# Performance work log

Measured on AMD Instinct MI355X. Metric: run time of the kernel, lower is better.

Reference implementation:

```python
import jax, jax.numpy as jnp
import numpy as np
import math

IN_C, OUT_C, KH, KW = 128, 128, 3, 3
GROUPS_NUM, NUM_W = 8, 8
STRIDE, PAD, DIL = 1, 1, 1
BETA = 1.0


def setup_inputs() -> dict:
    key = jax.random.key(0)
    ks = jax.random.split(key, 6)
    B, H, W = 8, 56, 56
    n = IN_C * KH * KW
    bound = math.sqrt(6.0 / n)  # reset_parameters bound for weight templates
    inputs = jax.random.normal(ks[0], (B, IN_C, H, W), jnp.float32)
    mask = jax.random.randint(ks[1], (B, H, W), 0, GROUPS_NUM)
    Alpha = jax.random.uniform(ks[2], (B, GROUPS_NUM, H, W), jnp.float32)
    weight_templates = jax.random.uniform(ks[3], (OUT_C * IN_C * KH * KW, NUM_W), jnp.float32, -bound, bound)
    routing_w = jax.random.normal(ks[4], (GROUPS_NUM * NUM_W, IN_C), jnp.float32) * 0.01
    routing_b = jnp.zeros((GROUPS_NUM * NUM_W,), jnp.float32)
    bias = jnp.zeros((OUT_C,), jnp.float32)
    return dict(inputs=inputs, mask=mask, Alpha=Alpha, weight_templates=weight_templates,
                routing_w=routing_w, routing_b=routing_b, bias=bias, use_alpha=1)


def _unfold(x):
    # torch F.unfold-compatible im2col: [B, C*KH*KW, Ho, Wo], channel-major feature order
    return jax.lax.conv_general_dilated_patches(
        x, (KH, KW), (STRIDE, STRIDE), [(PAD, PAD), (PAD, PAD)],
        rhs_dilation=(DIL, DIL), dimension_numbers=('NCHW', 'OIHW', 'NCHW'))


def reference(inputs, mask, Alpha, weight_templates, routing_w, routing_b, bias, use_alpha):
    B, C, H, W = inputs.shape
    K = IN_C * KH * KW
    # SE-style routing: GAP -> fc -> scaled sigmoid (alpha=1.0 in source)
    x_se = inputs.reshape(B, C, -1).mean(-1)                              # [B, C]
    x_se = 2.0 * jax.nn.sigmoid(x_se @ routing_w.T + routing_b) / NUM_W   # [B, G*num_W]
    # blend weight templates: F.linear(x_se.reshape(-1,num_W), weight)
    w = x_se.reshape(B * GROUPS_NUM, NUM_W) @ weight_templates.T          # [B*G, O*K]
    w = w.reshape(B, GROUPS_NUM, OUT_C, K).transpose(0, 2, 3, 1)          # [B, O, K, G]
    patches = _unfold(inputs)                                             # [B, K, Ho, Wo]
    # per-group convolution outputs, then per-pixel group routing
    y = jnp.einsum('bokg,bkhw->boghw', w, patches)                        # [B, O, G, Ho, Wo]
    if use_alpha:
        probs = jax.nn.softmax(BETA * Alpha, axis=1)                      # soft routing [B, G, Ho, Wo]
    else:
        probs = jax.nn.one_hot(mask, GROUPS_NUM, axis=1, dtype=y.dtype)   # hard per-pixel group select
    out = jnp.einsum('boghw,bghw->bohw', y, probs)
    return out + bias.reshape(1, -1, 1, 1)
```

## Files before the change

kernel.cpp:

```cpp
#include <hip/hip_runtime.h>
#include <stdint.h>

#define IN_C   128
#define OUT_C  128
#define KTOT   1152
#define NG     8
#define NW     8
#define NB     8
#define HH     56
#define WWID   56
#define NPIX   3136
#define PPAD   3200
#define MTOT   1024
#define HALO   58
#define HPIX   (HALO*HALO)


typedef __attribute__((ext_vector_type(8))) short short8;
typedef __attribute__((ext_vector_type(8))) unsigned short ushort8;
typedef __attribute__((ext_vector_type(4))) float f32x4;

__device__ __forceinline__ unsigned short f2bf(float f) {
    unsigned u = __float_as_uint(f);
    u += 0x7FFF + ((u >> 16) & 1);
    return (unsigned short)(u >> 16);
}

__device__ __forceinline__ void cp16(const unsigned short* g, unsigned short* l) {
    __builtin_amdgcn_global_load_lds(
        (const __attribute__((address_space(1))) unsigned int*)g,
        (__attribute__((address_space(3))) unsigned int*)l,
        16, 0, 0);
}

__global__ __launch_bounds__(256) void prep_kernel(const float* __restrict__ in,
                                                   const float* __restrict__ T,
                                                   float* __restrict__ xse,
                                                   unsigned short* __restrict__ Apack,
                                                   unsigned short* __restrict__ Xt) {
    __shared__ __align__(16) unsigned char smem[32768];
    const int blk = blockIdx.x;
    const int t = threadIdx.x;

    if (blk < 1024) {
        const float* src = in + (size_t)blk * NPIX;
        float s = 0.f;
        for (int i = t; i < NPIX / 4; i += 256) {
            float4 v = ((const float4*)src)[i];
            s += v.x + v.y + v.z + v.w;
        }
        #pragma unroll
        for (int off = 32; off; off >>= 1) s += __shfl_down(s, off);
        float* ws4 = (float*)smem;
        if ((t & 63) == 0) ws4[t >> 6] = s;
        __syncthreads();
        if (t == 0)
            xse[blk] = (ws4[0] + ws4[1] + ws4[2] + ws4[3]) * (1.0f / (float)NPIX);
        return;
    }
    if (blk < 1152) {
        unsigned short* lh = (unsigned short*)smem;
        const int o = blk - 1024;
        const float* To = T + (size_t)o * 9216;
        #pragma unroll
        for (int it = 0; it < 9; it++) {
            const int f = it * 256 + t;
            const float4 v = ((const float4*)To)[f];
            ushort4 h;
            h.x = f2bf(v.x); h.y = f2bf(v.y); h.z = f2bf(v.z); h.w = f2bf(v.w);
            *(ushort4*)&lh[f * 4] = h;
        }
        __syncthreads();
        const int m16b = o >> 1;
        const int lrb = (o & 1) * 8;
        #pragma unroll
        for (int it = 0; it < 5; it++) {
            const int ch = it * 256 + t;
            if (ch < 1152) {
                const int j = ch & 7, kc = ch >> 3;
                const int s = kc >> 4, c0 = (kc & 15) << 3;
                const int kt = kc >> 2, lq = kc & 3;
                ushort8 v;
                #pragma unroll
                for (int i = 0; i < 8; i++)
                    v[i] = lh[((c0 + i) * 9 + s) * 8 + j];
                const size_t off = ((((size_t)m16b * 36 + kt) * 4 + lq) * 16 + lrb + j) * 8;
                *(ushort8*)&Apack[off] = v;
            }
        }
        return;
    }
    unsigned short* tile = (unsigned short*)smem;
    const int idx = blk - 1152;
    const int yt = idx % 28;
    const int b  = idx / 28;
    const int y0 = yt * 2;

    #pragma unroll
    for (int it = 0; it < 14; it++) {
        const int f = it * 256 + t;
        const int c = f / 28;
        const int rem = f - c * 28;
        const int y = rem / 14;
        const int x4 = rem - y * 14;
        const float4 v = *(const float4*)(in + ((size_t)(b * IN_C + c)) * NPIX
                                          + (y0 + y) * WWID + x4 * 4);
        unsigned short bf0 = f2bf(v.x), bf1 = f2bf(v.y), bf2 = f2bf(v.z), bf3 = f2bf(v.w);
        const int ppb = (y * WWID + x4 * 4) ^ (((c >> 3) & 15) << 2);
        uint2 pk;
        pk.x = (unsigned)bf0 | ((unsigned)bf1 << 16);
        pk.y = (unsigned)bf2 | ((unsigned)bf3 << 16);
        *(uint2*)&tile[c * 128 + ppb] = pk;
    }
    __syncthreads();

    #pragma unroll
    for (int it = 0; it < 7; it++) {
        const int ch = it * 256 + t;
        const int oct = ch & 15;
        const int pp = ch >> 4;
        const int sw = oct << 2;
        ushort8 v;
        #pragma unroll
        for (int i = 0; i < 8; i++)
            v[i] = tile[(oct * 8 + i) * 128 + (pp ^ sw)];
        const int y2 = (pp >= WWID) ? 1 : 0;
        const int xg = pp - y2 * WWID;
        const size_t hp = (size_t)b * HPIX + (y0 + y2 + 1) * HALO + (xg + 1);
        *(ushort8*)&Xt[hp * 128 + oct * 8] = v;
    }

    if (t < 64) {
        const int pi = t >> 4, oct = t & 15;
        const int yy = y0 + 1 + (pi >> 1);
        const int xx = (pi & 1) * 57;
        *(ushort8*)&Xt[((size_t)b * HPIX + yy * HALO + xx) * 128 + oct * 8] =
            (ushort8){0, 0, 0, 0, 0, 0, 0, 0};
    }
    if (yt == 0 || yt == 27) {
        const int yy = (yt == 0) ? 0 : 57;
        #pragma unroll
        for (int it = 0; it < 4; it++) {
            const int ch = it * 256 + t;
            if (ch < 928) {
                const int xx = ch >> 4, oct = ch & 15;
                *(ushort8*)&Xt[((size_t)b * HPIX + yy * HALO + xx) * 128 + oct * 8] =
                    (ushort8){0, 0, 0, 0, 0, 0, 0, 0};
            }
        }
    }
}

__global__ __launch_bounds__(256) void s_kernel(const float* __restrict__ Alpha,
                                                const int* __restrict__ mask,
                                                const float* __restrict__ xse,
                                                const float* __restrict__ rw,
                                                const float* __restrict__ rb,
                                                const int* __restrict__ use_alpha,
                                                float* __restrict__ Sws) {
    const int b = blockIdx.y;
    const int t = threadIdx.x;
    const int p = blockIdx.x * 256 + t;
    __shared__ float xs[IN_C];
    __shared__ float rsh[64];
    if (t < IN_C) xs[t] = xse[b * IN_C + t];
    __syncthreads();
    if (t < 64) {
        float acc = rb[t];
        #pragma unroll 8
        for (int c = 0; c < IN_C; c++) acc += xs[c] * rw[t * IN_C + c];
        rsh[t] = 0.25f / (1.0f + expf(-acc));
    }
    __syncthreads();
    if (p >= PPAD) return;
    float sj[8] = {0, 0, 0, 0, 0, 0, 0, 0};
    if (p < NPIX) {
        float pr[8];
        if (use_alpha[0]) {
            float a[8], m = -1e30f;
            #pragma unroll
            for (int g = 0; g < 8; g++) {
                a[g] = Alpha[((size_t)(b * NG + g)) * NPIX + p];
                m = fmaxf(m, a[g]);
            }
            float sum = 0.f;
            #pragma unroll
            for (int g = 0; g < 8; g++) { pr[g] = expf(a[g] - m); sum += pr[g]; }
            float inv = 1.f / sum;
            #pragma unroll
            for (int g = 0; g < 8; g++) pr[g] *= inv;
        } else {
            int mg = mask[(size_t)b * NPIX + p];
            #pragma unroll
            for (int g = 0; g < 8; g++) pr[g] = (g == mg) ? 1.f : 0.f;
        }
        #pragma unroll
        for (int g = 0; g < 8; g++)
            #pragma unroll
            for (int j = 0; j < 8; j++) sj[j] += pr[g] * rsh[g * 8 + j];
    }
    float* dst = Sws + ((size_t)b * PPAD + p) * 8;
    *(f32x4*)dst = (f32x4){sj[0], sj[1], sj[2], sj[3]};
    *(f32x4*)(dst + 4) = (f32x4){sj[4], sj[5], sj[6], sj[7]};
}

__global__ __launch_bounds__(256) void gemm_kernel(const unsigned short* __restrict__ Apack,
                                                   const unsigned short* __restrict__ Xt,
                                                   const float* __restrict__ Sws,
                                                   const float* __restrict__ bias,
                                                   float* __restrict__ out) {
    __shared__ __align__(16) unsigned short Bsh[4][512 * 8];
    const int tid = threadIdx.x;
    const int wv = tid >> 6, ln = tid & 63;
    const int lq = ln >> 4, lr = ln & 15;
    const int wrow = wv >> 1, wcol = wv & 1;

    const int lid = blockIdx.x;
    const int b   = lid & 7;
    const int sl  = lid >> 3;
    const int mt  = sl & 15;
    const int nt  = sl >> 4;

    f32x4 acc[2][4];
    #pragma unroll
    for (int i = 0; i < 2; i++)
        #pragma unroll
        for (int j = 0; j < 4; j++) acc[i][j] = (f32x4){0.f, 0.f, 0.f, 0.f};

    const int js = tid & 3;
    const int r0 = tid >> 2,  q0 = js ^ (r0 & 3) ^ ((r0 >> 2) & 3);
    const int r1 = r0 + 64,   q1 = js ^ (r1 & 3) ^ ((r1 >> 2) & 3);
    const int p0 = min(nt * 128 + r0, NPIX - 1);
    const int p1 = min(nt * 128 + r1, NPIX - 1);
    const int y0p = p0 / WWID, x0p = p0 - y0p * WWID;
    const int y1p = p1 / WWID, x1p = p1 - y1p * WWID;
    const unsigned short* gb0 = Xt + ((size_t)b * HPIX + y0p * HALO + x0p) * 128 + q0 * 8;
    const unsigned short* gb1 = Xt + ((size_t)b * HPIX + y1p * HALO + x1p) * 128 + q1 * 8;
    unsigned short* lbA[4];
    #pragma unroll
    for (int i = 0; i < 4; i++) lbA[i] = &Bsh[i][(wv * 64) * 8];

    const unsigned short* gaw[2];
    #pragma unroll
    for (int tm = 0; tm < 2; tm++) {
        const int m16 = mt * 4 + wrow * 2 + tm;
        gaw[tm] = Apack + ((size_t)m16 * 36 * 64 + ln) * 8;
    }

    const int jj = lq ^ (lr & 3) ^ ((lr >> 2) & 3);

    cp16(gb0, lbA[0]); cp16(gb1, lbA[0] + 256 * 8);
    cp16(gb0 + 32, lbA[1]); cp16(gb1 + 32, lbA[1] + 256 * 8);
    short8 af[2][2];
    #pragma unroll
    for (int tm = 0; tm < 2; tm++) af[0][tm] = *(const short8*)(gaw[tm]);
    #pragma unroll
    for (int tm = 0; tm < 2; tm++) af[1][tm] = *(const short8*)(gaw[tm] + 512);

    #pragma unroll 1
    for (int pr = 0; pr < 18; pr++) {
        __syncthreads();
        const int st2 = pr * 2 + 2, st3 = pr * 2 + 3;
        if (pr < 17) {
            const int nk2 = st2 * 32, s2 = nk2 >> 7;
            const int kh2 = s2 / 3, kw2 = s2 - 3 * kh2;
            const int off2 = (kh2 * HALO + kw2) * 128 + (nk2 & 127);
            const int nk3 = st3 * 32, s3 = nk3 >> 7;
            const int kh3 = s3 / 3, kw3 = s3 - 3 * kh3;
            const int off3 = (kh3 * HALO + kw3) * 128 + (nk3 & 127);
            unsigned short* d2 = lbA[st2 & 3];
            unsigned short* d3 = lbA[st3 & 3];
            cp16(gb0 + off2, d2); cp16(gb1 + off2, d2 + 256 * 8);
            cp16(gb0 + off3, d3); cp16(gb1 + off3, d3 + 256 * 8);
        }
        const int bufa = (pr & 1) * 2;
        {
            short8 bfr[4];
            #pragma unroll
            for (int tn = 0; tn < 4; tn++) {
                const int row = wcol * 64 + tn * 16 + lr;
                bfr[tn] = *(const short8*)&Bsh[bufa][(row * 4 + jj) * 8];
            }
            #pragma unroll
            for (int tm = 0; tm < 2; tm++)
                #pragma unroll
                for (int tn = 0; tn < 4; tn++)
                    acc[tm][tn] = __builtin_amdgcn_mfma_f32_16x16x32_bf16(
                        af[0][tm], bfr[tn], acc[tm][tn], 0, 0, 0);
        }
        if (pr < 17) {
            #pragma unroll
            for (int tm = 0; tm < 2; tm++)
                af[0][tm] = *(const short8*)(gaw[tm] + (size_t)st2 * 512);
        }
        {
            short8 bfr[4];
            #pragma unroll
            for (int tn = 0; tn < 4; tn++) {
                const int row = wcol * 64 + tn * 16 + lr;
                bfr[tn] = *(const short8*)&Bsh[bufa + 1][(row * 4 + jj) * 8];
            }
            #pragma unroll
            for (int tm = 0; tm < 2; tm++)
                #pragma unroll
                for (int tn = 0; tn < 4; tn++)
                    acc[tm][tn] = __builtin_amdgcn_mfma_f32_16x16x32_bf16(
                        af[1][tm], bfr[tn], acc[tm][tn], 0, 0, 0);
        }
        if (pr < 17) {
            #pragma unroll
            for (int tm = 0; tm < 2; tm++)
                af[1][tm] = *(const short8*)(gaw[tm] + (size_t)st3 * 512);
        }
    }

    const int j0 = (lq & 1) * 4;
    const int oo = lq >> 1;
    #pragma unroll
    for (int tm = 0; tm < 2; tm++) {
        const int o = mt * 8 + wrow * 4 + tm * 2 + oo;
        const float bo = bias[o];
        #pragma unroll
        for (int tn = 0; tn < 4; tn++) {
            const int p = nt * 128 + wcol * 64 + tn * 16 + lr;
            const f32x4 sv = *(const f32x4*)&Sws[((size_t)b * PPAD + p) * 8 + j0];
            const f32x4 a = acc[tm][tn];
            float part = a.x * sv.x + a.y * sv.y + a.z * sv.z + a.w * sv.w;
            float tot = part + __shfl_xor(part, 16);
            if ((lq & 1) == 0 && p < NPIX)
                out[((size_t)b * OUT_C + o) * NPIX + p] = tot + bo;
        }
    }
}

extern "C" void kernel_launch(void* const* d_in, const int* in_sizes, int n_in,
                              void* d_out, int out_size, void* d_ws, size_t ws_size,
                              hipStream_t stream) {
    const float* inputs = (const float*)d_in[0];
    const int*   mask   = (const int*)d_in[1];
    const float* Alpha  = (const float*)d_in[2];
    const float* wtmpl  = (const float*)d_in[3];
    const float* rw     = (const float*)d_in[4];
    const float* rb     = (const float*)d_in[5];
    const float* bias   = (const float*)d_in[6];
    const int*   ua     = (const int*)d_in[7];
    float* out = (float*)d_out;

    char* ws = (char*)d_ws;
    unsigned short* Xt  = (unsigned short*)ws;
    unsigned short* Apk = (unsigned short*)(ws + 6889472);
    float*          Sws = (float*)(ws + 9248768);
    float*          xse = (float*)(ws + 10067968);

    prep_kernel<<<1376, 256, 0, stream>>>(inputs, wtmpl, xse, Apk, Xt);
    s_kernel<<<dim3(13, NB), 256, 0, stream>>>(Alpha, mask, xse, rw, rb, ua, Sws);
    gemm_kernel<<<3200, 256, 0, stream>>>(Apk, Xt, Sws, bias, out);
}
```

Baseline: 163.2 us.

## Switch GEMM to 32x32x16 MFMA with doubled M tile per block

Replaces the 16x16x32 bf16 MFMA tiles with 32x32x16 MFMA, repacks the weight matrix to match the new A-fragment layout, and doubles the M extent per block so the grid halves to 1600 blocks. Each B fragment loaded from LDS is now reused across a larger output tile, which lowers LDS read traffic per FLOP and the number of MFMA issues. The epilogue is rewritten for the 32x32 accumulator layout, and the Sws read index is clamped. The cost is more accumulator registers per wave and fewer blocks to spread across the CUs.

```diff
diff --git a/kernel.cpp b/kernel.cpp
--- a/kernel.cpp
+++ b/kernel.cpp
@@ -19,6 +19,7 @@
 typedef __attribute__((ext_vector_type(8))) short short8;
 typedef __attribute__((ext_vector_type(8))) unsigned short ushort8;
 typedef __attribute__((ext_vector_type(4))) float f32x4;
+typedef __attribute__((ext_vector_type(16))) float f32x16;
 
 __device__ __forceinline__ unsigned short f2bf(float f) {
     unsigned u = __float_as_uint(f);
@@ -71,20 +72,21 @@
             *(ushort4*)&lh[f * 4] = h;
         }
         __syncthreads();
-        const int m16b = o >> 1;
-        const int lrb = (o & 1) * 8;
         #pragma unroll
         for (int it = 0; it < 5; it++) {
             const int ch = it * 256 + t;
             if (ch < 1152) {
                 const int j = ch & 7, kc = ch >> 3;
                 const int s = kc >> 4, c0 = (kc & 15) << 3;
-                const int kt = kc >> 2, lq = kc & 3;
+                const int stg = s * 4 + ((c0 >> 5) & 3);
+                const int khb = (c0 >> 4) & 1;
+                const int hib = (c0 >> 3) & 1;
                 ushort8 v;
                 #pragma unroll
                 for (int i = 0; i < 8; i++)
                     v[i] = lh[((c0 + i) * 9 + s) * 8 + j];
-                const size_t off = ((((size_t)m16b * 36 + kt) * 4 + lq) * 16 + lrb + j) * 8;
+                const size_t off = ((((size_t)(o >> 2) * 36 + stg) * 2 + khb) * 64
+                                    + hib * 32 + (o & 3) * 8 + j) * 8;
                 *(ushort8*)&Apack[off] = v;
             }
         }
@@ -212,20 +214,22 @@
     __shared__ __align__(16) unsigned short Bsh[4][512 * 8];
     const int tid = threadIdx.x;
     const int wv = tid >> 6, ln = tid & 63;
-    const int lq = ln >> 4, lr = ln & 15;
+    const int u  = ln & 31, hi = ln >> 5;
     const int wrow = wv >> 1, wcol = wv & 1;
 
     const int lid = blockIdx.x;
     const int b   = lid & 7;
     const int sl  = lid >> 3;
-    const int mt  = sl & 15;
-    const int nt  = sl >> 4;
-
-    f32x4 acc[2][4];
+    const int mt  = sl & 7;
+    const int nt  = sl >> 3;
+
+    f32x16 acc[2][2];
     #pragma unroll
     for (int i = 0; i < 2; i++)
         #pragma unroll
-        for (int j = 0; j < 4; j++) acc[i][j] = (f32x4){0.f, 0.f, 0.f, 0.f};
+        for (int j = 0; j < 2; j++)
+            #pragma unroll
+            for (int e = 0; e < 16; e++) acc[i][j][e] = 0.f;
 
     const int js = tid & 3;
     const int r0 = tid >> 2,  q0 = js ^ (r0 & 3) ^ ((r0 >> 2) & 3);
@@ -240,22 +244,47 @@
     #pragma unroll
     for (int i = 0; i < 4; i++) lbA[i] = &Bsh[i][(wv * 64) * 8];
 
-    const unsigned short* gaw[2];
+    const unsigned short* gawB[2];
     #pragma unroll
     for (int tm = 0; tm < 2; tm++) {
-        const int m16 = mt * 4 + wrow * 2 + tm;
-        gaw[tm] = Apack + ((size_t)m16 * 36 * 64 + ln) * 8;
-    }
-
-    const int jj = lq ^ (lr & 3) ^ ((lr >> 2) & 3);
+        const int m32 = mt * 4 + wrow * 2 + tm;
+        gawB[tm] = Apack + (size_t)m32 * 36864 + ln * 8;
+    }
+
+    const int jbase = hi ^ (u & 3) ^ ((u >> 2) & 3);
+    int boffL[2][2];
+    #pragma unroll
+    for (int tn = 0; tn < 2; tn++)
+        #pragma unroll
+        for (int kh = 0; kh < 2; kh++) {
+            const int row = wcol * 64 + tn * 32 + u;
+            boffL[tn][kh] = (row * 4 + (jbase ^ (kh << 1))) * 8;
+        }
+
+#define ALOAD(Ad, st_) { _Pragma("unroll")                                    \
+        for (int tm_ = 0; tm_ < 2; tm_++) { _Pragma("unroll")                 \
+            for (int kh_ = 0; kh_ < 2; kh_++)                                 \
+                Ad[tm_][kh_] = *(const short8*)(gawB[tm_] + (st_) * 1024 + kh_ * 512); } }
+
+#define STAGE(Ad, buf_) {                                                     \
+        short8 b0 = *(const short8*)&Bsh[buf_][boffL[0][0]];                  \
+        short8 b1 = *(const short8*)&Bsh[buf_][boffL[1][0]];                  \
+        acc[0][0] = __builtin_amdgcn_mfma_f32_32x32x16_bf16(Ad[0][0], b0, acc[0][0], 0, 0, 0); \
+        acc[0][1] = __builtin_amdgcn_mfma_f32_32x32x16_bf16(Ad[0][0], b1, acc[0][1], 0, 0, 0); \
+        acc[1][0] = __builtin_amdgcn_mfma_f32_32x32x16_bf16(Ad[1][0], b0, acc[1][0], 0, 0, 0); \
+        acc[1][1] = __builtin_amdgcn_mfma_f32_32x32x16_bf16(Ad[1][0], b1, acc[1][1], 0, 0, 0); \
+        b0 = *(const short8*)&Bsh[buf_][boffL[0][1]];                         \
+        b1 = *(const short8*)&Bsh[buf_][boffL[1][1]];                         \
+        acc[0][0] = __builtin_amdgcn_mfma_f32_32x32x16_bf16(Ad[0][1], b0, acc[0][0], 0, 0, 0); \
+        acc[0][1] = __builtin_amdgcn_mfma_f32_32x32x16_bf16(Ad[0][1], b1, acc[0][1], 0, 0, 0); \
+        acc[1][0] = __builtin_amdgcn_mfma_f32_32x32x16_bf16(Ad[1][1], b0, acc[1][0], 0, 0, 0); \
+        acc[1][1] = __builtin_amdgcn_mfma_f32_32x32x16_bf16(Ad[1][1], b1, acc[1][1], 0, 0, 0); }
 
     cp16(gb0, lbA[0]); cp16(gb1, lbA[0] + 256 * 8);
     cp16(gb0 + 32, lbA[1]); cp16(gb1 + 32, lbA[1] + 256 * 8);
-    short8 af[2][2];
-    #pragma unroll
-    for (int tm = 0; tm < 2; tm++) af[0][tm] = *(const short8*)(gaw[tm]);
-    #pragma unroll
-    for (int tm = 0; tm < 2; tm++) af[1][tm] = *(const short8*)(gaw[tm] + 512);
+    short8 A0[2][2], A1[2][2];
+    ALOAD(A0, 0);
+    ALOAD(A1, 1);
 
     #pragma unroll 1
     for (int pr = 0; pr < 18; pr++) {
@@ -274,61 +303,33 @@
             cp16(gb0 + off3, d3); cp16(gb1 + off3, d3 + 256 * 8);
         }
         const int bufa = (pr & 1) * 2;
-        {
-            short8 bfr[4];
-            #pragma unroll
-            for (int tn = 0; tn < 4; tn++) {
-                const int row = wcol * 64 + tn * 16 + lr;
-                bfr[tn] = *(const short8*)&Bsh[bufa][(row * 4 + jj) * 8];
+        STAGE(A0, bufa);
+        if (pr < 17) ALOAD(A0, st2);
+        STAGE(A1, bufa + 1);
+        if (pr < 17) ALOAD(A1, st3);
+    }
+#undef STAGE
+#undef ALOAD
+
+    const int j0 = hi * 4;
+    #pragma unroll
+    for (int tm = 0; tm < 2; tm++) {
+        const int m32 = mt * 4 + wrow * 2 + tm;
+        #pragma unroll
+        for (int tn = 0; tn < 2; tn++) {
+            const int p = nt * 128 + wcol * 64 + tn * 32 + u;
+            const int pS = min(p, NPIX - 1);
+            const f32x4 sv = *(const f32x4*)&Sws[((size_t)b * PPAD + pS) * 8 + j0];
+            const f32x16 a = acc[tm][tn];
+            #pragma unroll
+            for (int q = 0; q < 4; q++) {
+                float part = a[q * 4 + 0] * sv.x + a[q * 4 + 1] * sv.y
+                           + a[q * 4 + 2] * sv.z + a[q * 4 + 3] * sv.w;
+                float tot = part + __shfl_xor(part, 32);
+                const int o = m32 * 4 + q;
+                if (hi == 0 && p < NPIX)
+                    out[((size_t)(b * OUT_C + o)) * NPIX + p] = tot + bias[o];
             }
-            #pragma unroll
-            for (int tm = 0; tm < 2; tm++)
-                #pragma unroll
-                for (int tn = 0; tn < 4; tn++)
-                    acc[tm][tn] = __builtin_amdgcn_mfma_f32_16x16x32_bf16(
-                        af[0][tm], bfr[tn], acc[tm][tn], 0, 0, 0);
-        }
-        if (pr < 17) {
-            #pragma unroll
-            for (int tm = 0; tm < 2; tm++)
-                af[0][tm] = *(const short8*)(gaw[tm] + (size_t)st2 * 512);
-        }
-        {
-            short8 bfr[4];
-            #pragma unroll
-            for (int tn = 0; tn < 4; tn++) {
-                const int row = wcol * 64 + tn * 16 + lr;
-                bfr[tn] = *(const short8*)&Bsh[bufa + 1][(row * 4 + jj) * 8];
-            }
-            #pragma unroll
-            for (int tm = 0; tm < 2; tm++)
-                #pragma unroll
-                for (int tn = 0; tn < 4; tn++)
-                    acc[tm][tn] = __builtin_amdgcn_mfma_f32_16x16x32_bf16(
-                        af[1][tm], bfr[tn], acc[tm][tn], 0, 0, 0);
-        }
-        if (pr < 17) {
-            #pragma unroll
-            for (int tm = 0; tm < 2; tm++)
-                af[1][tm] = *(const short8*)(gaw[tm] + (size_t)st3 * 512);
-        }
-    }
-
-    const int j0 = (lq & 1) * 4;
-    const int oo = lq >> 1;
-    #pragma unroll
-    for (int tm = 0; tm < 2; tm++) {
-        const int o = mt * 8 + wrow * 4 + tm * 2 + oo;
-        const float bo = bias[o];
-        #pragma unroll
-        for (int tn = 0; tn < 4; tn++) {
-            const int p = nt * 128 + wcol * 64 + tn * 16 + lr;
-            const f32x4 sv = *(const f32x4*)&Sws[((size_t)b * PPAD + p) * 8 + j0];
-            const f32x4 a = acc[tm][tn];
-            float part = a.x * sv.x + a.y * sv.y + a.z * sv.z + a.w * sv.w;
-            float tot = part + __shfl_xor(part, 16);
-            if ((lq & 1) == 0 && p < NPIX)
-                out[((size_t)b * OUT_C + o) * NPIX + p] = tot + bo;
         }
     }
 }
@@ -354,5 +355,5 @@
 
     prep_kernel<<<1376, 256, 0, stream>>>(inputs, wtmpl, xse, Apk, Xt);
     s_kernel<<<dim3(13, NB), 256, 0, stream>>>(Alpha, mask, xse, rw, rb, ua, Sws);
-    gemm_kernel<<<3200, 256, 0, stream>>>(Apk, Xt, Sws, bias, out);
-}
+    gemm_kernel<<<1600, 256, 0, stream>>>(Apk, Xt, Sws, bias, out);
+}
```

Result: slower. 171.8 us (+5.3%).
